# Kernel optimization log

Measured on AMD Instinct MI355X. Metric: run time of the kernel, lower is better.

The kernel has to match this reference:

```python
import jax, jax.numpy as jnp
import numpy as np
import math

N = 20000      # nodes
E = 640000     # edges (avg degree 32)
G = 128        # g_dim (input features)
H1 = 128       # rgcn output dim
H2 = 128       # transformer output dim
R = 8          # num_relations


def setup_inputs() -> dict:
    key = jax.random.key(0)
    ks = jax.random.split(key, 12)
    x = jax.random.normal(ks[0], (N, G), dtype=jnp.float32)
    edge_index = jax.random.randint(ks[1], (2, E), 0, N)
    edge_type = jax.random.randint(ks[2], (E,), 0, R)
    s_in = 1.0 / math.sqrt(G)
    s_h1 = 1.0 / math.sqrt(H1)
    return {
        'x': x,
        'edge_index': edge_index,
        'edge_type': edge_type,
        # RGCNConv params (per-relation weights + root weight + bias)
        'rgcn_weight': jax.random.normal(ks[3], (R, G, H1), dtype=jnp.float32) * s_in,
        'rgcn_root': jax.random.normal(ks[4], (G, H1), dtype=jnp.float32) * s_in,
        'rgcn_bias': jnp.zeros((H1,), dtype=jnp.float32),
        # TransformerConv params (heads=1): query/key/value + skip linear
        'Wq': jax.random.normal(ks[5], (H1, H2), dtype=jnp.float32) * s_h1,
        'bq': jnp.zeros((H2,), dtype=jnp.float32),
        'Wk': jax.random.normal(ks[6], (H1, H2), dtype=jnp.float32) * s_h1,
        'bk': jnp.zeros((H2,), dtype=jnp.float32),
        'Wv': jax.random.normal(ks[7], (H1, H2), dtype=jnp.float32) * s_h1,
        'bv': jnp.zeros((H2,), dtype=jnp.float32),
        'Ws': jax.random.normal(ks[8], (H1, H2), dtype=jnp.float32) * s_h1,
        'bs': jnp.zeros((H2,), dtype=jnp.float32),
    }


def reference(x, edge_index, edge_type, rgcn_weight, rgcn_root, rgcn_bias,
              Wq, bq, Wk, bk, Wv, bv, Ws, bs):
    n = x.shape[0]
    src, dst = edge_index[0], edge_index[1]

    # ---- RGCNConv (aggr='mean' per relation, root weight + bias) ----
    # transform nodes by every relation, then gather per-edge message
    xr = jnp.einsum('ni,rio->nro', x, rgcn_weight)          # [N, R, H1]
    msg = xr[src, edge_type]                                # [E, H1]
    # per (dst, relation) edge counts for mean aggregation
    cnt = jnp.zeros((n, rgcn_weight.shape[0]), x.dtype).at[dst, edge_type].add(1.0)
    denom = jnp.maximum(cnt[dst, edge_type], 1.0)[:, None]  # [E, 1]
    agg = jnp.zeros((n, rgcn_weight.shape[2]), x.dtype).at[dst].add(msg / denom)
    h = agg + x @ rgcn_root + rgcn_bias
    h = jax.nn.relu(h)

    # ---- TransformerConv (heads=1, concat, root_weight=True) ----
    d = Wq.shape[1]
    q = h @ Wq + bq                                          # [N, H2]
    k = h @ Wk + bk
    v = h @ Wv + bv
    score = jnp.sum(q[dst] * k[src], axis=-1) / math.sqrt(d) # [E]
    # softmax over incoming edges of each destination node
    smax = jax.ops.segment_max(score, dst, num_segments=n)   # [N]
    e = jnp.exp(score - smax[dst])                           # [E]
    den = jax.ops.segment_sum(e, dst, num_segments=n)        # [N]
    alpha = e / jnp.maximum(den[dst], 1e-16)                 # [E]
    out = jax.ops.segment_sum(alpha[:, None] * v[src], dst, num_segments=n)
    out = out + h @ Ws + bs                                  # skip connection
    return jax.nn.relu(out)
```

## Files before the change

kernel.cpp:

```cpp
#include <hip/hip_runtime.h>

typedef unsigned short u16;
typedef unsigned int u32;
typedef __attribute__((ext_vector_type(8))) short short8;
typedef __attribute__((ext_vector_type(4))) float f32x4;

#define NN 20000
#define EE 640000
#define SCAN_BLOCKS 80

__device__ inline u16 f2bf(float f) {
    u32 x = __float_as_uint(f);
    return (u16)((x + 0x7FFFu + ((x >> 16) & 1u)) >> 16);
}
__device__ inline float lo16(u32 w) { return __uint_as_float(w << 16); }
__device__ inline float hi16(u32 w) { return __uint_as_float(w & 0xFFFF0000u); }
__device__ inline u32 packbf(float a, float b) { return ((u32)f2bf(b) << 16) | (u32)f2bf(a); }

#define CT_N (EE / 8)
#define CX_N (NN * 32)
#define WP_N (128 * 1152 + 4 * 128 * 128 + 512)
__global__ __launch_bounds__(256) void prep_count(const int* __restrict__ ei,
                                                  const int* __restrict__ et,
                                                  int* __restrict__ cnt, int* __restrict__ rank,
                                                  const float* __restrict__ x,
                                                  const float* rw, const float* root,
                                                  const float* Wq, const float* Wk,
                                                  const float* Wv, const float* Ws,
                                                  const float* bq, const float* bk,
                                                  const float* bv, const float* bs,
                                                  u16* __restrict__ xb, u16* __restrict__ pre,
                                                  u16* wt1, u16* wt2, float* bcat) {
    int idx = blockIdx.x * 256 + threadIdx.x;
    if (idx < CT_N) {
#pragma unroll
        for (int j = 0; j < 8; j++) {
            int e = idx + j * CT_N;
            int dst = ei[EE + e];
            int r = et[e];
            rank[e] = atomicAdd(&cnt[dst * 8 + r], 1);
        }
        return;
    }
    idx -= CT_N;
    if (idx < CX_N) {
        float4 v = *(const float4*)(x + (size_t)idx * 4);
        uint2 o;
        o.x = packbf(v.x, v.y);
        o.y = packbf(v.z, v.w);
        *(uint2*)(xb + (size_t)idx * 4) = o;
        int node = idx >> 5;
        int d = (idx & 31) * 4;
        *(uint2*)(pre + (long)node * 1152 + 1024 + d) = o;
        return;
    }
    idx -= CX_N;
    const int S1 = 128 * 1152, S2 = 4 * 128 * 128;
    if (idx < S1) {
        int o = idx / 1152, k = idx - o * 1152;
        float v = (k < 1024) ? rw[k * 128 + o] : root[(k - 1024) * 128 + o];
        wt1[idx] = f2bf(v);
    } else if (idx < S1 + S2) {
        int j = idx - S1;
        int y = j >> 14, rem = j & 16383, o = rem >> 7, i = rem & 127;
        const float* W = (y == 0) ? Wq : (y == 1) ? Wk : (y == 2) ? Wv : Ws;
        wt2[j] = f2bf(W[i * 128 + o]);
    } else if (idx < S1 + S2 + 512) {
        int j = idx - (S1 + S2);
        int y = j >> 7, c = j & 127;
        const float* b = (y == 0) ? bq : (y == 1) ? bk : (y == 2) ? bv : bs;
        bcat[j] = b[c];
    }
}

__global__ __launch_bounds__(256) void scan_phase1(const int* __restrict__ cnt,
                                                   int* __restrict__ deg_pref,
                                                   int* __restrict__ blk_sums) {
    __shared__ int lds[256];
    int t = threadIdx.x;
    int n = blockIdx.x * 256 + t;
    int d = 0;
    if (n < NN) {
        int4 c0 = *(const int4*)(cnt + n * 8);
        int4 c1 = *(const int4*)(cnt + n * 8 + 4);
        d = c0.x + c0.y + c0.z + c0.w + c1.x + c1.y + c1.z + c1.w;
    }
    lds[t] = d;
    __syncthreads();
    for (int o = 1; o < 256; o <<= 1) {
        int v = (t >= o) ? lds[t - o] : 0;
        __syncthreads();
        lds[t] += v;
        __syncthreads();
    }
    if (n < NN) deg_pref[n] = lds[t];
    if (t == 255) blk_sums[blockIdx.x] = lds[255];
}

__global__ __launch_bounds__(256) void scan_phase3(const int* __restrict__ cnt,
                                                   const int* __restrict__ deg_pref,
                                                   const int* __restrict__ blk_sums,
                                                   int* __restrict__ row_off,
                                                   int* __restrict__ srt) {
    __shared__ int bs_lds[128];
    int t = threadIdx.x;
    if (t < 128) {
        int v = (t < SCAN_BLOCKS) ? blk_sums[t] : 0;
        bs_lds[t] = v;
    }
    __syncthreads();
    if (t < 128) {
        for (int o = 1; o < 128; o <<= 1) {
            int a = (t >= o) ? bs_lds[t - o] : 0;
            __syncthreads();
            bs_lds[t] += a;
            __syncthreads();
        }
    } else {
        for (int o = 1; o < 128; o <<= 1) {
            __syncthreads();
            __syncthreads();
        }
    }
    int blk_excl = (blockIdx.x > 0) ? bs_lds[blockIdx.x - 1] : 0;
    int n = blockIdx.x * 256 + t;
    if (n >= NN) return;
    int4 c0 = *(const int4*)(cnt + n * 8);
    int4 c1 = *(const int4*)(cnt + n * 8 + 4);
    int deg = c0.x + c0.y + c0.z + c0.w + c1.x + c1.y + c1.z + c1.w;
    int start = blk_excl + deg_pref[n] - deg;
    row_off[n] = start;
    int sub = start;
    int o[8];
    o[0] = sub; sub += c0.x;
    o[1] = sub; sub += c0.y;
    o[2] = sub; sub += c0.z;
    o[3] = sub; sub += c0.w;
    o[4] = sub; sub += c1.x;
    o[5] = sub; sub += c1.y;
    o[6] = sub; sub += c1.z;
    o[7] = sub; sub += c1.w;
    *(int4*)(srt + n * 8) = make_int4(o[0], o[1], o[2], o[3]);
    *(int4*)(srt + n * 8 + 4) = make_int4(o[4], o[5], o[6], o[7]);
    if (n == NN - 1) row_off[NN] = sub;
}

__global__ void scatter_kernel(const int* __restrict__ ei, const int* __restrict__ et,
                               const int* __restrict__ srt, const int* __restrict__ rank,
                               int* __restrict__ es) {
    int base = blockIdx.x * 2048 + threadIdx.x;
#pragma unroll
    for (int j = 0; j < 8; j++) {
        int e = base + j * 256;
        if (e < EE) {
            int dst = ei[EE + e];
            int src = ei[e];
            int r = et[e];
            es[srt[dst * 8 + r] + rank[e]] = src;
        }
    }
}

__global__ __launch_bounds__(256) void rgcn_agg(const u16* __restrict__ xb,
                                                const int* __restrict__ srt,
                                                const int* __restrict__ cnt,
                                                const int* __restrict__ es,
                                                u16* __restrict__ pre) {
    int gid = blockIdx.x * 16 + (threadIdx.x >> 4);
    int lane = threadIdx.x & 15;
    if (gid >= NN * 8) return;
    int node = gid >> 3;
    int slot = gid & 7;
    int c = cnt[node * 8 + slot];
    int p0 = srt[node * 8 + slot];
    float inv = 1.0f / (float)(c > 1 ? c : 1);
    float a0 = 0.f, a1 = 0.f, a2 = 0.f, a3 = 0.f, a4 = 0.f, a5 = 0.f, a6 = 0.f, a7 = 0.f;
    int i = 0;
    for (; i + 4 <= c; i += 4) {
        int s0 = es[p0 + i], s1 = es[p0 + i + 1], s2 = es[p0 + i + 2], s3 = es[p0 + i + 3];
        uint4 w0 = *(const uint4*)(xb + (long)s0 * 128 + lane * 8);
        uint4 w1 = *(const uint4*)(xb + (long)s1 * 128 + lane * 8);
        uint4 w2 = *(const uint4*)(xb + (long)s2 * 128 + lane * 8);
        uint4 w3 = *(const uint4*)(xb + (long)s3 * 128 + lane * 8);
        a0 += (lo16(w0.x) + lo16(w1.x)) + (lo16(w2.x) + lo16(w3.x));
        a1 += (hi16(w0.x) + hi16(w1.x)) + (hi16(w2.x) + hi16(w3.x));
        a2 += (lo16(w0.y) + lo16(w1.y)) + (lo16(w2.y) + lo16(w3.y));
        a3 += (hi16(w0.y) + hi16(w1.y)) + (hi16(w2.y) + hi16(w3.y));
        a4 += (lo16(w0.z) + lo16(w1.z)) + (lo16(w2.z) + lo16(w3.z));
        a5 += (hi16(w0.z) + hi16(w1.z)) + (hi16(w2.z) + hi16(w3.z));
        a6 += (lo16(w0.w) + lo16(w1.w)) + (lo16(w2.w) + lo16(w3.w));
        a7 += (hi16(w0.w) + hi16(w1.w)) + (hi16(w2.w) + hi16(w3.w));
    }
    for (; i < c; i++) {
        int s = es[p0 + i];
        uint4 w = *(const uint4*)(xb + (long)s * 128 + lane * 8);
        a0 += lo16(w.x); a1 += hi16(w.x); a2 += lo16(w.y); a3 += hi16(w.y);
        a4 += lo16(w.z); a5 += hi16(w.z); a6 += lo16(w.w); a7 += hi16(w.w);
    }
    uint4 ow;
    ow.x = packbf(a0 * inv, a1 * inv);
    ow.y = packbf(a2 * inv, a3 * inv);
    ow.z = packbf(a4 * inv, a5 * inv);
    ow.w = packbf(a6 * inv, a7 * inv);
    *(uint4*)(pre + (long)node * 1152 + slot * 128 + lane * 8) = ow;
}

__global__ __launch_bounds__(256) void gemm_fused(const u16* __restrict__ A,
                                                  const u16* __restrict__ Bt1,
                                                  const float* __restrict__ bias1,
                                                  const u16* __restrict__ Wt2,
                                                  const float* __restrict__ bcat,
                                                  u16* __restrict__ Cq, u16* __restrict__ Ckv,
                                                  u16* __restrict__ Cs) {
    __shared__ u16 As[32 * 136];
    __shared__ u16 Bs[128 * 136];
    int tid = threadIdx.x;
    int w = tid >> 6;
    int lane = tid & 63;
    int quad = lane >> 4;
    int ml = lane & 15;
    int mt = w & 1;
    int nq = w >> 1;
    int block_m = blockIdx.x * 32;

    f32x4 acc[4];
#pragma unroll
    for (int i = 0; i < 4; i++) acc[i] = (f32x4){0.f, 0.f, 0.f, 0.f};

    int rbase = tid >> 4;
    int cb = (tid & 15) * 8;

    for (int kb = 0; kb < 1152; kb += 128) {
#pragma unroll
        for (int rep = 0; rep < 2; rep++) {
            int r = rbase + rep * 16;
            short8 val = *(const short8*)(A + (long)(block_m + r) * 1152 + kb + cb);
            *(short8*)(As + r * 136 + cb) = val;
        }
#pragma unroll
        for (int rep = 0; rep < 8; rep++) {
            int r = rbase + rep * 16;
            short8 val = *(const short8*)(Bt1 + (long)r * 1152 + kb + cb);
            *(short8*)(Bs + r * 136 + cb) = val;
        }
        __syncthreads();
#pragma unroll
        for (int ks = 0; ks < 4; ks++) {
            short8 af = *(const short8*)(As + (mt * 16 + ml) * 136 + ks * 32 + quad * 8);
#pragma unroll
            for (int nt = 0; nt < 4; nt++) {
                short8 bfr = *(const short8*)(Bs + (nq * 64 + nt * 16 + ml) * 136 + ks * 32 + quad * 8);
                acc[nt] = __builtin_amdgcn_mfma_f32_16x16x32_bf16(af, bfr, acc[nt], 0, 0, 0);
            }
        }
        __syncthreads();
    }
#pragma unroll
    for (int nt = 0; nt < 4; nt++) {
        int col = nq * 64 + nt * 16 + ml;
        float bv = bias1[col];
#pragma unroll
        for (int i = 0; i < 4; i++) {
            int r = mt * 16 + quad * 4 + i;
            As[r * 136 + col] = f2bf(fmaxf(acc[nt][i] + bv, 0.f));
        }
    }
    __syncthreads();

#pragma unroll 1
    for (int y = 0; y < 4; y++) {
#pragma unroll
        for (int rep = 0; rep < 8; rep++) {
            int r = rbase + rep * 16;
            short8 val = *(const short8*)(Wt2 + (long)y * 16384 + (long)r * 128 + cb);
            *(short8*)(Bs + r * 136 + cb) = val;
        }
        __syncthreads();
        f32x4 acc2[4];
#pragma unroll
        for (int i = 0; i < 4; i++) acc2[i] = (f32x4){0.f, 0.f, 0.f, 0.f};
#pragma unroll
        for (int ks = 0; ks < 4; ks++) {
            short8 af = *(const short8*)(As + (mt * 16 + ml) * 136 + ks * 32 + quad * 8);
#pragma unroll
            for (int nt = 0; nt < 4; nt++) {
                short8 bfr = *(const short8*)(Bs + (nq * 64 + nt * 16 + ml) * 136 + ks * 32 + quad * 8);
                acc2[nt] = __builtin_amdgcn_mfma_f32_16x16x32_bf16(af, bfr, acc2[nt], 0, 0, 0);
            }
        }
        u16* C;
        int ldc;
        if (y == 0) { C = Cq; ldc = 128; }
        else if (y == 1) { C = Ckv; ldc = 256; }
        else if (y == 2) { C = Ckv + 128; ldc = 256; }
        else { C = Cs; ldc = 128; }
#pragma unroll
        for (int nt = 0; nt < 4; nt++) {
            int col = nq * 64 + nt * 16 + ml;
            float bv = bcat[y * 128 + col];
#pragma unroll
            for (int i = 0; i < 4; i++) {
                int gr = block_m + mt * 16 + quad * 4 + i;
                C[(long)gr * ldc + col] = f2bf(acc2[nt][i] + bv);
            }
        }
        __syncthreads();
    }
}

__global__ __launch_bounds__(128) void attn_kernel(const u16* __restrict__ q,
                                                   const u16* __restrict__ kv,
                                                   const u16* __restrict__ skip,
                                                   const int* __restrict__ row_off,
                                                   const int* __restrict__ es,
                                                   float* __restrict__ out) {
    int node = blockIdx.x * 8 + (threadIdx.x >> 4);
    int lane = threadIdx.x & 15;
    if (node >= NN) return;
    int p0 = row_off[node], p1 = row_off[node + 1];
    uint4 qw = *(const uint4*)(q + (long)node * 128 + lane * 8);
    float q0 = lo16(qw.x), q1 = hi16(qw.x), q2 = lo16(qw.y), q3 = hi16(qw.y);
    float q4 = lo16(qw.z), q5 = hi16(qw.z), q6 = lo16(qw.w), q7 = hi16(qw.w);
    const float SC = 0.08838834764831845f;
    float l = 0.f;
    float a0 = 0.f, a1 = 0.f, a2 = 0.f, a3 = 0.f, a4 = 0.f, a5 = 0.f, a6 = 0.f, a7 = 0.f;
    int p = p0;
    for (; p + 4 <= p1; p += 4) {
        const u16* b0 = kv + (long)es[p] * 256 + lane * 8;
        const u16* b1 = kv + (long)es[p + 1] * 256 + lane * 8;
        const u16* b2 = kv + (long)es[p + 2] * 256 + lane * 8;
        const u16* b3 = kv + (long)es[p + 3] * 256 + lane * 8;
        uint4 k0 = *(const uint4*)b0;
        uint4 k1 = *(const uint4*)b1;
        uint4 k2 = *(const uint4*)b2;
        uint4 k3 = *(const uint4*)b3;
        uint4 v0 = *(const uint4*)(b0 + 128);
        uint4 v1 = *(const uint4*)(b1 + 128);
        uint4 v2 = *(const uint4*)(b2 + 128);
        uint4 v3 = *(const uint4*)(b3 + 128);
        float t0 = q0 * lo16(k0.x) + q1 * hi16(k0.x) + q2 * lo16(k0.y) + q3 * hi16(k0.y) +
                   q4 * lo16(k0.z) + q5 * hi16(k0.z) + q6 * lo16(k0.w) + q7 * hi16(k0.w);
        float t1 = q0 * lo16(k1.x) + q1 * hi16(k1.x) + q2 * lo16(k1.y) + q3 * hi16(k1.y) +
                   q4 * lo16(k1.z) + q5 * hi16(k1.z) + q6 * lo16(k1.w) + q7 * hi16(k1.w);
        float t2 = q0 * lo16(k2.x) + q1 * hi16(k2.x) + q2 * lo16(k2.y) + q3 * hi16(k2.y) +
                   q4 * lo16(k2.z) + q5 * hi16(k2.z) + q6 * lo16(k2.w) + q7 * hi16(k2.w);
        float t3 = q0 * lo16(k3.x) + q1 * hi16(k3.x) + q2 * lo16(k3.y) + q3 * hi16(k3.y) +
                   q4 * lo16(k3.z) + q5 * hi16(k3.z) + q6 * lo16(k3.w) + q7 * hi16(k3.w);
#pragma unroll
        for (int off = 8; off >= 1; off >>= 1) {
            t0 += __shfl_xor(t0, off, 16);
            t1 += __shfl_xor(t1, off, 16);
            t2 += __shfl_xor(t2, off, 16);
            t3 += __shfl_xor(t3, off, 16);
        }
        float w0 = __expf(fminf(t0 * SC, 70.f));
        float w1 = __expf(fminf(t1 * SC, 70.f));
        float w2 = __expf(fminf(t2 * SC, 70.f));
        float w3 = __expf(fminf(t3 * SC, 70.f));
        l += (w0 + w1) + (w2 + w3);
        a0 += w0 * lo16(v0.x) + w1 * lo16(v1.x) + w2 * lo16(v2.x) + w3 * lo16(v3.x);
        a1 += w0 * hi16(v0.x) + w1 * hi16(v1.x) + w2 * hi16(v2.x) + w3 * hi16(v3.x);
        a2 += w0 * lo16(v0.y) + w1 * lo16(v1.y) + w2 * lo16(v2.y) + w3 * lo16(v3.y);
        a3 += w0 * hi16(v0.y) + w1 * hi16(v1.y) + w2 * hi16(v2.y) + w3 * hi16(v3.y);
        a4 += w0 * lo16(v0.z) + w1 * lo16(v1.z) + w2 * lo16(v2.z) + w3 * lo16(v3.z);
        a5 += w0 * hi16(v0.z) + w1 * hi16(v1.z) + w2 * hi16(v2.z) + w3 * hi16(v3.z);
        a6 += w0 * lo16(v0.w) + w1 * lo16(v1.w) + w2 * lo16(v2.w) + w3 * lo16(v3.w);
        a7 += w0 * hi16(v0.w) + w1 * hi16(v1.w) + w2 * hi16(v2.w) + w3 * hi16(v3.w);
    }
    for (; p < p1; p++) {
        const u16* b = kv + (long)es[p] * 256 + lane * 8;
        uint4 kw = *(const uint4*)b;
        uint4 vw = *(const uint4*)(b + 128);
        float t = q0 * lo16(kw.x) + q1 * hi16(kw.x) + q2 * lo16(kw.y) + q3 * hi16(kw.y) +
                  q4 * lo16(kw.z) + q5 * hi16(kw.z) + q6 * lo16(kw.w) + q7 * hi16(kw.w);
#pragma unroll
        for (int off = 8; off >= 1; off >>= 1) t += __shfl_xor(t, off, 16);
        float w = __expf(fminf(t * SC, 70.f));
        l += w;
        a0 += w * lo16(vw.x);
        a1 += w * hi16(vw.x);
        a2 += w * lo16(vw.y);
        a3 += w * hi16(vw.y);
        a4 += w * lo16(vw.z);
        a5 += w * hi16(vw.z);
        a6 += w * lo16(vw.w);
        a7 += w * hi16(vw.w);
    }
    float invl = (l > 0.f) ? 1.0f / l : 0.f;
    uint4 sw = *(const uint4*)(skip + (long)node * 128 + lane * 8);
    float4 oa, ob;
    oa.x = fmaxf(a0 * invl + lo16(sw.x), 0.f);
    oa.y = fmaxf(a1 * invl + hi16(sw.x), 0.f);
    oa.z = fmaxf(a2 * invl + lo16(sw.y), 0.f);
    oa.w = fmaxf(a3 * invl + hi16(sw.y), 0.f);
    ob.x = fmaxf(a4 * invl + lo16(sw.z), 0.f);
    ob.y = fmaxf(a5 * invl + hi16(sw.z), 0.f);
    ob.z = fmaxf(a6 * invl + lo16(sw.w), 0.f);
    ob.w = fmaxf(a7 * invl + hi16(sw.w), 0.f);
    *(float4*)(out + (long)node * 128 + lane * 8) = oa;
    *(float4*)(out + (long)node * 128 + lane * 8 + 4) = ob;
}

extern "C" void kernel_launch(void* const* d_in, const int* in_sizes, int n_in,
                              void* d_out, int out_size, void* d_ws, size_t ws_size,
                              hipStream_t stream) {
    const float* x = (const float*)d_in[0];
    const int* ei = (const int*)d_in[1];
    const int* et = (const int*)d_in[2];
    const float* rw = (const float*)d_in[3];
    const float* root = (const float*)d_in[4];
    const float* rbias = (const float*)d_in[5];
    const float* Wq = (const float*)d_in[6];
    const float* bq = (const float*)d_in[7];
    const float* Wk = (const float*)d_in[8];
    const float* bk = (const float*)d_in[9];
    const float* Wv = (const float*)d_in[10];
    const float* bv = (const float*)d_in[11];
    const float* Ws = (const float*)d_in[12];
    const float* bs = (const float*)d_in[13];

    char* ws = (char*)d_ws;
    size_t off = 0;
    auto alloc = [&](size_t b) {
        size_t o = off;
        off = (off + b + 255) & ~(size_t)255;
        return o;
    };
    u16* pre = (u16*)(ws + alloc((size_t)NN * 1152 * 2));
    u16* qv = (u16*)(ws + alloc((size_t)NN * 128 * 2));
    u16* kv = (u16*)(ws + alloc((size_t)NN * 256 * 2));
    u16* skip = (u16*)(ws + alloc((size_t)NN * 128 * 2));
    u16* xb = (u16*)(ws + alloc((size_t)NN * 128 * 2));
    u16* wt1 = (u16*)(ws + alloc((size_t)128 * 1152 * 2));
    u16* wt2 = (u16*)(ws + alloc((size_t)4 * 128 * 128 * 2));
    float* bcat = (float*)(ws + alloc((size_t)512 * 4));
    int* cnt = (int*)(ws + alloc((size_t)NN * 8 * 4));
    int* row_off = (int*)(ws + alloc((size_t)(NN + 1) * 4));
    int* srt = (int*)(ws + alloc((size_t)NN * 8 * 4));
    int* deg_pref = (int*)(ws + alloc((size_t)NN * 4));
    int* blk_sums = (int*)(ws + alloc((size_t)128 * 4));
    int* rank = (int*)(ws + alloc((size_t)EE * 4));
    int* es = (int*)(ws + alloc((size_t)EE * 4));
    (void)ws_size;
    (void)in_sizes;
    (void)n_in;
    (void)out_size;

    hipMemsetAsync(cnt, 0, (size_t)NN * 8 * 4, stream);

    prep_count<<<(CT_N + CX_N + WP_N + 255) / 256, 256, 0, stream>>>(
        ei, et, cnt, rank, x, rw, root, Wq, Wk, Wv, Ws, bq, bk, bv, bs,
        xb, pre, wt1, wt2, bcat);

    scan_phase1<<<SCAN_BLOCKS, 256, 0, stream>>>(cnt, deg_pref, blk_sums);
    scan_phase3<<<SCAN_BLOCKS, 256, 0, stream>>>(cnt, deg_pref, blk_sums, row_off, srt);
    scatter_kernel<<<(EE + 2047) / 2048, 256, 0, stream>>>(ei, et, srt, rank, es);

    rgcn_agg<<<(NN * 8 + 15) / 16, 256, 0, stream>>>(xb, srt, cnt, es, pre);

    gemm_fused<<<NN / 32, 256, 0, stream>>>(pre, wt1, rbias, wt2, bcat, qv, kv, skip);

    attn_kernel<<<(NN + 7) / 8, 128, 0, stream>>>(qv, kv, skip, row_off, es, (float*)d_out);
}
```

Before: 232.6 us.

## Merge scan and scatter into a cooperative kernel; double GEMM M-tile to 64

The two scan kernels and the edge scatter become one cooperative kernel that separates its phases with grid-wide syncs, removing two kernel launches and their gaps. The fused GEMM now computes 64 rows per block instead of 32, with two A fragments per warp. Each weight tile loaded into shared memory is therefore reused across twice as many rows, halving weight traffic per output. In exchange the grid shrinks to 313 blocks, which lowers occupancy on a device with many CUs. The last block also loads A rows past NN without a bounds check; only its stores are guarded.

Result: slower. 365.7 us (+57.2%).

```diff
diff --git a/kernel.cpp b/kernel.cpp
--- a/kernel.cpp
+++ b/kernel.cpp
@@ -1,4 +1,5 @@
 #include <hip/hip_runtime.h>
+#include <hip/hip_cooperative_groups.h>
 
 typedef unsigned short u16;
 typedef unsigned int u32;
@@ -8,6 +9,7 @@
 #define NN 20000
 #define EE 640000
 #define SCAN_BLOCKS 80
+#define COOP_BLOCKS 512
 
 __device__ inline u16 f2bf(float f) {
     u32 x = __float_as_uint(f);
@@ -73,91 +75,82 @@
     }
 }
 
-__global__ __launch_bounds__(256) void scan_phase1(const int* __restrict__ cnt,
-                                                   int* __restrict__ deg_pref,
-                                                   int* __restrict__ blk_sums) {
+__global__ __launch_bounds__(256, 2) void sort_coop(const int* __restrict__ ei,
+                                                    const int* __restrict__ et,
+                                                    const int* __restrict__ cnt,
+                                                    const int* __restrict__ rank,
+                                                    int* __restrict__ deg_pref,
+                                                    int* __restrict__ blk_sums,
+                                                    int* __restrict__ row_off,
+                                                    int* __restrict__ srt,
+                                                    int* __restrict__ es) {
+    cooperative_groups::grid_group grid = cooperative_groups::this_grid();
     __shared__ int lds[256];
-    int t = threadIdx.x;
-    int n = blockIdx.x * 256 + t;
-    int d = 0;
-    if (n < NN) {
-        int4 c0 = *(const int4*)(cnt + n * 8);
-        int4 c1 = *(const int4*)(cnt + n * 8 + 4);
-        d = c0.x + c0.y + c0.z + c0.w + c1.x + c1.y + c1.z + c1.w;
-    }
-    lds[t] = d;
-    __syncthreads();
-    for (int o = 1; o < 256; o <<= 1) {
-        int v = (t >= o) ? lds[t - o] : 0;
-        __syncthreads();
-        lds[t] += v;
-        __syncthreads();
-    }
-    if (n < NN) deg_pref[n] = lds[t];
-    if (t == 255) blk_sums[blockIdx.x] = lds[255];
-}
-
-__global__ __launch_bounds__(256) void scan_phase3(const int* __restrict__ cnt,
-                                                   const int* __restrict__ deg_pref,
-                                                   const int* __restrict__ blk_sums,
-                                                   int* __restrict__ row_off,
-                                                   int* __restrict__ srt) {
     __shared__ int bs_lds[128];
     int t = threadIdx.x;
-    if (t < 128) {
-        int v = (t < SCAN_BLOCKS) ? blk_sums[t] : 0;
-        bs_lds[t] = v;
-    }
-    __syncthreads();
-    if (t < 128) {
+    int b = blockIdx.x;
+
+    if (b < SCAN_BLOCKS) {
+        int n = b * 256 + t;
+        int d = 0;
+        if (n < NN) {
+            int4 c0 = *(const int4*)(cnt + n * 8);
+            int4 c1 = *(const int4*)(cnt + n * 8 + 4);
+            d = c0.x + c0.y + c0.z + c0.w + c1.x + c1.y + c1.z + c1.w;
+        }
+        lds[t] = d;
+        __syncthreads();
+        for (int o = 1; o < 256; o <<= 1) {
+            int v = (t >= o) ? lds[t - o] : 0;
+            __syncthreads();
+            lds[t] += v;
+            __syncthreads();
+        }
+        if (n < NN) deg_pref[n] = lds[t];
+        if (t == 255) blk_sums[b] = lds[255];
+    }
+    grid.sync();
+
+    if (b < SCAN_BLOCKS) {
+        if (t < 128) bs_lds[t] = (t < SCAN_BLOCKS) ? blk_sums[t] : 0;
+        __syncthreads();
         for (int o = 1; o < 128; o <<= 1) {
-            int a = (t >= o) ? bs_lds[t - o] : 0;
+            int a = (t < 128 && t >= o) ? bs_lds[t - o] : 0;
             __syncthreads();
-            bs_lds[t] += a;
+            if (t < 128 && t >= o) bs_lds[t] += a;
             __syncthreads();
         }
-    } else {
-        for (int o = 1; o < 128; o <<= 1) {
-            __syncthreads();
-            __syncthreads();
-        }
-    }
-    int blk_excl = (blockIdx.x > 0) ? bs_lds[blockIdx.x - 1] : 0;
-    int n = blockIdx.x * 256 + t;
-    if (n >= NN) return;
-    int4 c0 = *(const int4*)(cnt + n * 8);
-    int4 c1 = *(const int4*)(cnt + n * 8 + 4);
-    int deg = c0.x + c0.y + c0.z + c0.w + c1.x + c1.y + c1.z + c1.w;
-    int start = blk_excl + deg_pref[n] - deg;
-    row_off[n] = start;
-    int sub = start;
-    int o[8];
-    o[0] = sub; sub += c0.x;
-    o[1] = sub; sub += c0.y;
-    o[2] = sub; sub += c0.z;
-    o[3] = sub; sub += c0.w;
-    o[4] = sub; sub += c1.x;
-    o[5] = sub; sub += c1.y;
-    o[6] = sub; sub += c1.z;
-    o[7] = sub; sub += c1.w;
-    *(int4*)(srt + n * 8) = make_int4(o[0], o[1], o[2], o[3]);
-    *(int4*)(srt + n * 8 + 4) = make_int4(o[4], o[5], o[6], o[7]);
-    if (n == NN - 1) row_off[NN] = sub;
-}
-
-__global__ void scatter_kernel(const int* __restrict__ ei, const int* __restrict__ et,
-                               const int* __restrict__ srt, const int* __restrict__ rank,
-                               int* __restrict__ es) {
-    int base = blockIdx.x * 2048 + threadIdx.x;
-#pragma unroll
-    for (int j = 0; j < 8; j++) {
-        int e = base + j * 256;
-        if (e < EE) {
-            int dst = ei[EE + e];
-            int src = ei[e];
-            int r = et[e];
-            es[srt[dst * 8 + r] + rank[e]] = src;
-        }
+        int blk_excl = (b > 0) ? bs_lds[b - 1] : 0;
+        int n = b * 256 + t;
+        if (n < NN) {
+            int4 c0 = *(const int4*)(cnt + n * 8);
+            int4 c1 = *(const int4*)(cnt + n * 8 + 4);
+            int deg = c0.x + c0.y + c0.z + c0.w + c1.x + c1.y + c1.z + c1.w;
+            int start = blk_excl + deg_pref[n] - deg;
+            row_off[n] = start;
+            int sub = start;
+            int o2[8];
+            o2[0] = sub; sub += c0.x;
+            o2[1] = sub; sub += c0.y;
+            o2[2] = sub; sub += c0.z;
+            o2[3] = sub; sub += c0.w;
+            o2[4] = sub; sub += c1.x;
+            o2[5] = sub; sub += c1.y;
+            o2[6] = sub; sub += c1.z;
+            o2[7] = sub; sub += c1.w;
+            *(int4*)(srt + n * 8) = make_int4(o2[0], o2[1], o2[2], o2[3]);
+            *(int4*)(srt + n * 8 + 4) = make_int4(o2[4], o2[5], o2[6], o2[7]);
+            if (n == NN - 1) row_off[NN] = sub;
+        }
+    }
+    grid.sync();
+
+    const int stride = COOP_BLOCKS * 256;
+    for (int e = b * 256 + t; e < EE; e += stride) {
+        int dst = ei[EE + e];
+        int src = ei[e];
+        int r = et[e];
+        es[srt[dst * 8 + r] + rank[e]] = src;
     }
 }
 
@@ -212,7 +205,7 @@
                                                   const float* __restrict__ bcat,
                                                   u16* __restrict__ Cq, u16* __restrict__ Ckv,
                                                   u16* __restrict__ Cs) {
-    __shared__ u16 As[32 * 136];
+    __shared__ u16 As[64 * 136];
     __shared__ u16 Bs[128 * 136];
     int tid = threadIdx.x;
     int w = tid >> 6;
@@ -221,18 +214,20 @@
     int ml = lane & 15;
     int mt = w & 1;
     int nq = w >> 1;
-    int block_m = blockIdx.x * 32;
-
-    f32x4 acc[4];
-#pragma unroll
-    for (int i = 0; i < 4; i++) acc[i] = (f32x4){0.f, 0.f, 0.f, 0.f};
+    int block_m = blockIdx.x * 64;
+
+    f32x4 acc[2][4];
+#pragma unroll
+    for (int m = 0; m < 2; m++)
+#pragma unroll
+        for (int i = 0; i < 4; i++) acc[m][i] = (f32x4){0.f, 0.f, 0.f, 0.f};
 
     int rbase = tid >> 4;
     int cb = (tid & 15) * 8;
 
     for (int kb = 0; kb < 1152; kb += 128) {
 #pragma unroll
-        for (int rep = 0; rep < 2; rep++) {
+        for (int rep = 0; rep < 4; rep++) {
             int r = rbase + rep * 16;
             short8 val = *(const short8*)(A + (long)(block_m + r) * 1152 + kb + cb);
             *(short8*)(As + r * 136 + cb) = val;
@@ -246,25 +241,29 @@
         __syncthreads();
 #pragma unroll
         for (int ks = 0; ks < 4; ks++) {
-            short8 af = *(const short8*)(As + (mt * 16 + ml) * 136 + ks * 32 + quad * 8);
+            short8 af0 = *(const short8*)(As + (mt * 32 + ml) * 136 + ks * 32 + quad * 8);
+            short8 af1 = *(const short8*)(As + (mt * 32 + 16 + ml) * 136 + ks * 32 + quad * 8);
 #pragma unroll
             for (int nt = 0; nt < 4; nt++) {
                 short8 bfr = *(const short8*)(Bs + (nq * 64 + nt * 16 + ml) * 136 + ks * 32 + quad * 8);
-                acc[nt] = __builtin_amdgcn_mfma_f32_16x16x32_bf16(af, bfr, acc[nt], 0, 0, 0);
+                acc[0][nt] = __builtin_amdgcn_mfma_f32_16x16x32_bf16(af0, bfr, acc[0][nt], 0, 0, 0);
+                acc[1][nt] = __builtin_amdgcn_mfma_f32_16x16x32_bf16(af1, bfr, acc[1][nt], 0, 0, 0);
             }
         }
         __syncthreads();
     }
 #pragma unroll
-    for (int nt = 0; nt < 4; nt++) {
-        int col = nq * 64 + nt * 16 + ml;
-        float bv = bias1[col];
-#pragma unroll
-        for (int i = 0; i < 4; i++) {
-            int r = mt * 16 + quad * 4 + i;
-            As[r * 136 + col] = f2bf(fmaxf(acc[nt][i] + bv, 0.f));
-        }
-    }
+    for (int mfr = 0; mfr < 2; mfr++)
+#pragma unroll
+        for (int nt = 0; nt < 4; nt++) {
+            int col = nq * 64 + nt * 16 + ml;
+            float bv = bias1[col];
+#pragma unroll
+            for (int i = 0; i < 4; i++) {
+                int r = mt * 32 + mfr * 16 + quad * 4 + i;
+                As[r * 136 + col] = f2bf(fmaxf(acc[mfr][nt][i] + bv, 0.f));
+            }
+        }
     __syncthreads();
 
 #pragma unroll 1
@@ -276,16 +275,20 @@
             *(short8*)(Bs + r * 136 + cb) = val;
         }
         __syncthreads();
-        f32x4 acc2[4];
-#pragma unroll
-        for (int i = 0; i < 4; i++) acc2[i] = (f32x4){0.f, 0.f, 0.f, 0.f};
+        f32x4 acc2[2][4];
+#pragma unroll
+        for (int m = 0; m < 2; m++)
+#pragma unroll
+            for (int i = 0; i < 4; i++) acc2[m][i] = (f32x4){0.f, 0.f, 0.f, 0.f};
 #pragma unroll
         for (int ks = 0; ks < 4; ks++) {
-            short8 af = *(const short8*)(As + (mt * 16 + ml) * 136 + ks * 32 + quad * 8);
+            short8 af0 = *(const short8*)(As + (mt * 32 + ml) * 136 + ks * 32 + quad * 8);
+            short8 af1 = *(const short8*)(As + (mt * 32 + 16 + ml) * 136 + ks * 32 + quad * 8);
 #pragma unroll
             for (int nt = 0; nt < 4; nt++) {
                 short8 bfr = *(const short8*)(Bs + (nq * 64 + nt * 16 + ml) * 136 + ks * 32 + quad * 8);
-                acc2[nt] = __builtin_amdgcn_mfma_f32_16x16x32_bf16(af, bfr, acc2[nt], 0, 0, 0);
+                acc2[0][nt] = __builtin_amdgcn_mfma_f32_16x16x32_bf16(af0, bfr, acc2[0][nt], 0, 0, 0);
+                acc2[1][nt] = __builtin_amdgcn_mfma_f32_16x16x32_bf16(af1, bfr, acc2[1][nt], 0, 0, 0);
             }
         }
         u16* C;
@@ -295,15 +298,17 @@
         else if (y == 2) { C = Ckv + 128; ldc = 256; }
         else { C = Cs; ldc = 128; }
 #pragma unroll
-        for (int nt = 0; nt < 4; nt++) {
-            int col = nq * 64 + nt * 16 + ml;
-            float bv = bcat[y * 128 + col];
-#pragma unroll
-            for (int i = 0; i < 4; i++) {
-                int gr = block_m + mt * 16 + quad * 4 + i;
-                C[(long)gr * ldc + col] = f2bf(acc2[nt][i] + bv);
+        for (int mfr = 0; mfr < 2; mfr++)
+#pragma unroll
+            for (int nt = 0; nt < 4; nt++) {
+                int col = nq * 64 + nt * 16 + ml;
+                float bv = bcat[y * 128 + col];
+#pragma unroll
+                for (int i = 0; i < 4; i++) {
+                    int gr = block_m + mt * 32 + mfr * 16 + quad * 4 + i;
+                    if (gr < NN) C[(long)gr * ldc + col] = f2bf(acc2[mfr][nt][i] + bv);
+                }
             }
-        }
         __syncthreads();
     }
 }
@@ -452,13 +457,17 @@
         ei, et, cnt, rank, x, rw, root, Wq, Wk, Wv, Ws, bq, bk, bv, bs,
         xb, pre, wt1, wt2, bcat);
 
-    scan_phase1<<<SCAN_BLOCKS, 256, 0, stream>>>(cnt, deg_pref, blk_sums);
-    scan_phase3<<<SCAN_BLOCKS, 256, 0, stream>>>(cnt, deg_pref, blk_sums, row_off, srt);
-    scatter_kernel<<<(EE + 2047) / 2048, 256, 0, stream>>>(ei, et, srt, rank, es);
+    {
+        void* args[] = {(void*)&ei, (void*)&et, (void*)&cnt, (void*)&rank,
+                        (void*)&deg_pref, (void*)&blk_sums, (void*)&row_off,
+                        (void*)&srt, (void*)&es};
+        hipLaunchCooperativeKernel((void*)sort_coop, dim3(COOP_BLOCKS), dim3(256),
+                                   args, 0, stream);
+    }
 
     rgcn_agg<<<(NN * 8 + 15) / 16, 256, 0, stream>>>(xb, srt, cnt, es, pre);
 
-    gemm_fused<<<NN / 32, 256, 0, stream>>>(pre, wt1, rbias, wt2, bcat, qv, kv, skip);
+    gemm_fused<<<(NN + 63) / 64, 256, 0, stream>>>(pre, wt1, rbias, wt2, bcat, qv, kv, skip);
 
     attn_kernel<<<(NN + 7) / 8, 128, 0, stream>>>(qv, kv, skip, row_off, es, (float*)d_out);
 }
```

## Fuse RGCN mean aggregation into GEMM A-tile loading, drop pre buffer

Applied to the files above, without the earlier changes.

Removes the separate rgcn_agg kernel and the NN×1152 bf16 intermediate buffer. The GEMM kernel now builds each 32-row by 128-column A tile in shared memory by gathering and averaging neighbor features for each relation slot, and uses xb directly for the root slot. This saves a large global write and read plus a kernel launch. In exchange the irregular gather latency now sits inside the GEMM loop, and only 625 blocks of 8 threads per node do it, so there is less parallelism to hide gather latency.

New measurement: 233.8 us. Within noise of the previous version (+0.5%).

```diff
diff --git a/kernel.cpp b/kernel.cpp
--- a/kernel.cpp
+++ b/kernel.cpp
@@ -29,7 +29,7 @@
                                                   const float* Wv, const float* Ws,
                                                   const float* bq, const float* bk,
                                                   const float* bv, const float* bs,
-                                                  u16* __restrict__ xb, u16* __restrict__ pre,
+                                                  u16* __restrict__ xb,
                                                   u16* wt1, u16* wt2, float* bcat) {
     int idx = blockIdx.x * 256 + threadIdx.x;
     if (idx < CT_N) {
@@ -49,9 +49,6 @@
         o.x = packbf(v.x, v.y);
         o.y = packbf(v.z, v.w);
         *(uint2*)(xb + (size_t)idx * 4) = o;
-        int node = idx >> 5;
-        int d = (idx & 31) * 4;
-        *(uint2*)(pre + (long)node * 1152 + 1024 + d) = o;
         return;
     }
     idx -= CX_N;
@@ -161,57 +158,16 @@
     }
 }
 
-__global__ __launch_bounds__(256) void rgcn_agg(const u16* __restrict__ xb,
-                                                const int* __restrict__ srt,
-                                                const int* __restrict__ cnt,
-                                                const int* __restrict__ es,
-                                                u16* __restrict__ pre) {
-    int gid = blockIdx.x * 16 + (threadIdx.x >> 4);
-    int lane = threadIdx.x & 15;
-    if (gid >= NN * 8) return;
-    int node = gid >> 3;
-    int slot = gid & 7;
-    int c = cnt[node * 8 + slot];
-    int p0 = srt[node * 8 + slot];
-    float inv = 1.0f / (float)(c > 1 ? c : 1);
-    float a0 = 0.f, a1 = 0.f, a2 = 0.f, a3 = 0.f, a4 = 0.f, a5 = 0.f, a6 = 0.f, a7 = 0.f;
-    int i = 0;
-    for (; i + 4 <= c; i += 4) {
-        int s0 = es[p0 + i], s1 = es[p0 + i + 1], s2 = es[p0 + i + 2], s3 = es[p0 + i + 3];
-        uint4 w0 = *(const uint4*)(xb + (long)s0 * 128 + lane * 8);
-        uint4 w1 = *(const uint4*)(xb + (long)s1 * 128 + lane * 8);
-        uint4 w2 = *(const uint4*)(xb + (long)s2 * 128 + lane * 8);
-        uint4 w3 = *(const uint4*)(xb + (long)s3 * 128 + lane * 8);
-        a0 += (lo16(w0.x) + lo16(w1.x)) + (lo16(w2.x) + lo16(w3.x));
-        a1 += (hi16(w0.x) + hi16(w1.x)) + (hi16(w2.x) + hi16(w3.x));
-        a2 += (lo16(w0.y) + lo16(w1.y)) + (lo16(w2.y) + lo16(w3.y));
-        a3 += (hi16(w0.y) + hi16(w1.y)) + (hi16(w2.y) + hi16(w3.y));
-        a4 += (lo16(w0.z) + lo16(w1.z)) + (lo16(w2.z) + lo16(w3.z));
-        a5 += (hi16(w0.z) + hi16(w1.z)) + (hi16(w2.z) + hi16(w3.z));
-        a6 += (lo16(w0.w) + lo16(w1.w)) + (lo16(w2.w) + lo16(w3.w));
-        a7 += (hi16(w0.w) + hi16(w1.w)) + (hi16(w2.w) + hi16(w3.w));
-    }
-    for (; i < c; i++) {
-        int s = es[p0 + i];
-        uint4 w = *(const uint4*)(xb + (long)s * 128 + lane * 8);
-        a0 += lo16(w.x); a1 += hi16(w.x); a2 += lo16(w.y); a3 += hi16(w.y);
-        a4 += lo16(w.z); a5 += hi16(w.z); a6 += lo16(w.w); a7 += hi16(w.w);
-    }
-    uint4 ow;
-    ow.x = packbf(a0 * inv, a1 * inv);
-    ow.y = packbf(a2 * inv, a3 * inv);
-    ow.z = packbf(a4 * inv, a5 * inv);
-    ow.w = packbf(a6 * inv, a7 * inv);
-    *(uint4*)(pre + (long)node * 1152 + slot * 128 + lane * 8) = ow;
-}
-
-__global__ __launch_bounds__(256) void gemm_fused(const u16* __restrict__ A,
-                                                  const u16* __restrict__ Bt1,
-                                                  const float* __restrict__ bias1,
-                                                  const u16* __restrict__ Wt2,
-                                                  const float* __restrict__ bcat,
-                                                  u16* __restrict__ Cq, u16* __restrict__ Ckv,
-                                                  u16* __restrict__ Cs) {
+__global__ __launch_bounds__(256) void gemm_rgcn_fused(const u16* __restrict__ xb,
+                                                       const int* __restrict__ srt,
+                                                       const int* __restrict__ cnt,
+                                                       const int* __restrict__ es,
+                                                       const u16* __restrict__ Bt1,
+                                                       const float* __restrict__ bias1,
+                                                       const u16* __restrict__ Wt2,
+                                                       const float* __restrict__ bcat,
+                                                       u16* __restrict__ Cq, u16* __restrict__ Ckv,
+                                                       u16* __restrict__ Cs) {
     __shared__ u16 As[32 * 136];
     __shared__ u16 Bs[128 * 136];
     int tid = threadIdx.x;
@@ -223,25 +179,79 @@
     int nq = w >> 1;
     int block_m = blockIdx.x * 32;
 
-    f32x4 acc[4];
-#pragma unroll
-    for (int i = 0; i < 4; i++) acc[i] = (f32x4){0.f, 0.f, 0.f, 0.f};
-
     int rbase = tid >> 4;
     int cb = (tid & 15) * 8;
 
-    for (int kb = 0; kb < 1152; kb += 128) {
-#pragma unroll
-        for (int rep = 0; rep < 2; rep++) {
-            int r = rbase + rep * 16;
-            short8 val = *(const short8*)(A + (long)(block_m + r) * 1152 + kb + cb);
-            *(short8*)(As + r * 136 + cb) = val;
-        }
+    int node_l = tid >> 3;
+    int th = tid & 7;
+    int db = th * 16;
+    int gnode = block_m + node_l;
+
+    f32x4 acc[4];
+#pragma unroll
+    for (int i = 0; i < 4; i++) acc[i] = (f32x4){0.f, 0.f, 0.f, 0.f};
+
+#pragma unroll 1
+    for (int slot = 0; slot < 9; slot++) {
+        int kb = slot * 128;
 #pragma unroll
         for (int rep = 0; rep < 8; rep++) {
             int r = rbase + rep * 16;
             short8 val = *(const short8*)(Bt1 + (long)r * 1152 + kb + cb);
             *(short8*)(Bs + r * 136 + cb) = val;
+        }
+        if (slot < 8) {
+            int c = cnt[gnode * 8 + slot];
+            int p0 = srt[gnode * 8 + slot];
+            float a0 = 0.f, a1 = 0.f, a2 = 0.f, a3 = 0.f, a4 = 0.f, a5 = 0.f, a6 = 0.f, a7 = 0.f;
+            float a8 = 0.f, a9 = 0.f, a10 = 0.f, a11 = 0.f, a12 = 0.f, a13 = 0.f, a14 = 0.f, a15 = 0.f;
+            int i = 0;
+            for (; i + 2 <= c; i += 2) {
+                int s0 = es[p0 + i], s1 = es[p0 + i + 1];
+                uint4 wa0 = *(const uint4*)(xb + (long)s0 * 128 + db);
+                uint4 wa1 = *(const uint4*)(xb + (long)s0 * 128 + db + 8);
+                uint4 wb0 = *(const uint4*)(xb + (long)s1 * 128 + db);
+                uint4 wb1 = *(const uint4*)(xb + (long)s1 * 128 + db + 8);
+                a0 += lo16(wa0.x) + lo16(wb0.x);
+                a1 += hi16(wa0.x) + hi16(wb0.x);
+                a2 += lo16(wa0.y) + lo16(wb0.y);
+                a3 += hi16(wa0.y) + hi16(wb0.y);
+                a4 += lo16(wa0.z) + lo16(wb0.z);
+                a5 += hi16(wa0.z) + hi16(wb0.z);
+                a6 += lo16(wa0.w) + lo16(wb0.w);
+                a7 += hi16(wa0.w) + hi16(wb0.w);
+                a8 += lo16(wa1.x) + lo16(wb1.x);
+                a9 += hi16(wa1.x) + hi16(wb1.x);
+                a10 += lo16(wa1.y) + lo16(wb1.y);
+                a11 += hi16(wa1.y) + hi16(wb1.y);
+                a12 += lo16(wa1.z) + lo16(wb1.z);
+                a13 += hi16(wa1.z) + hi16(wb1.z);
+                a14 += lo16(wa1.w) + lo16(wb1.w);
+                a15 += hi16(wa1.w) + hi16(wb1.w);
+            }
+            if (i < c) {
+                int s0 = es[p0 + i];
+                uint4 wa0 = *(const uint4*)(xb + (long)s0 * 128 + db);
+                uint4 wa1 = *(const uint4*)(xb + (long)s0 * 128 + db + 8);
+                a0 += lo16(wa0.x); a1 += hi16(wa0.x); a2 += lo16(wa0.y); a3 += hi16(wa0.y);
+                a4 += lo16(wa0.z); a5 += hi16(wa0.z); a6 += lo16(wa0.w); a7 += hi16(wa0.w);
+                a8 += lo16(wa1.x); a9 += hi16(wa1.x); a10 += lo16(wa1.y); a11 += hi16(wa1.y);
+                a12 += lo16(wa1.z); a13 += hi16(wa1.z); a14 += lo16(wa1.w); a15 += hi16(wa1.w);
+            }
+            float inv = 1.0f / (float)(c > 1 ? c : 1);
+            uint4 o0 = make_uint4(packbf(a0 * inv, a1 * inv), packbf(a2 * inv, a3 * inv),
+                                  packbf(a4 * inv, a5 * inv), packbf(a6 * inv, a7 * inv));
+            uint4 o1 = make_uint4(packbf(a8 * inv, a9 * inv), packbf(a10 * inv, a11 * inv),
+                                  packbf(a12 * inv, a13 * inv), packbf(a14 * inv, a15 * inv));
+            *(uint4*)(As + node_l * 136 + db) = o0;
+            *(uint4*)(As + node_l * 136 + db + 8) = o1;
+        } else {
+#pragma unroll
+            for (int rep = 0; rep < 2; rep++) {
+                int r = rbase + rep * 16;
+                short8 val = *(const short8*)(xb + (long)(block_m + r) * 128 + cb);
+                *(short8*)(As + r * 136 + cb) = val;
+            }
         }
         __syncthreads();
 #pragma unroll
@@ -426,7 +436,6 @@
         off = (off + b + 255) & ~(size_t)255;
         return o;
     };
-    u16* pre = (u16*)(ws + alloc((size_t)NN * 1152 * 2));
     u16* qv = (u16*)(ws + alloc((size_t)NN * 128 * 2));
     u16* kv = (u16*)(ws + alloc((size_t)NN * 256 * 2));
     u16* skip = (u16*)(ws + alloc((size_t)NN * 128 * 2));
@@ -450,15 +459,14 @@
 
     prep_count<<<(CT_N + CX_N + WP_N + 255) / 256, 256, 0, stream>>>(
         ei, et, cnt, rank, x, rw, root, Wq, Wk, Wv, Ws, bq, bk, bv, bs,
-        xb, pre, wt1, wt2, bcat);
+        xb, wt1, wt2, bcat);
 
     scan_phase1<<<SCAN_BLOCKS, 256, 0, stream>>>(cnt, deg_pref, blk_sums);
     scan_phase3<<<SCAN_BLOCKS, 256, 0, stream>>>(cnt, deg_pref, blk_sums, row_off, srt);
     scatter_kernel<<<(EE + 2047) / 2048, 256, 0, stream>>>(ei, et, srt, rank, es);
 
-    rgcn_agg<<<(NN * 8 + 15) / 16, 256, 0, stream>>>(xb, srt, cnt, es, pre);
-
-    gemm_fused<<<NN / 32, 256, 0, stream>>>(pre, wt1, rbias, wt2, bcat, qv, kv, skip);
+    gemm_rgcn_fused<<<NN / 32, 256, 0, stream>>>(xb, srt, cnt, es, wt1, rbias, wt2, bcat,
+                                                 qv, kv, skip);
 
     attn_kernel<<<(NN + 7) / 8, 128, 0, stream>>>(qv, kv, skip, row_off, es, (float*)d_out);
 }
```
